# Optimization experiments

Hardware: AMD Instinct MI355X
Metric: run time of the kernel (lower is better)

Reference implementation:

```python
import jax, jax.numpy as jnp
import numpy as np

HEADS = 16
D_MODEL = 1024
EXPANSION = 2
D_EXP = D_MODEL * EXPANSION          # 2048
D_HEAD = D_EXP // HEADS              # 128
B, SEQ = 1, 2048
LN_EPS = 1e-5
NEG_BIG = -1e10


def layer_norm(x, w, b):
    mu = jnp.mean(x, axis=-1, keepdims=True)
    var = jnp.var(x, axis=-1, keepdims=True)
    return (x - mu) * jax.lax.rsqrt(var + LN_EPS) * w + b


def setup_inputs() -> dict:
    key = jax.random.key(0)
    ks = jax.random.split(key, 8)
    d_out = 4 * D_EXP + HEADS  # merged fanout linear: q,k,v,p (D_EXP each) + y (HEADS)
    x = jax.random.normal(ks[0], (B, SEQ, D_MODEL), dtype=jnp.float32)
    W_in = 0.02 * jax.random.normal(ks[1], (d_out, D_MODEL), dtype=jnp.float32)
    b_in = jnp.zeros((d_out,), dtype=jnp.float32)
    # position head init from module: weight zeros, bias linspace(-8,8,heads)
    W_in = W_in.at[4 * D_EXP:].set(0.0)
    b_in = b_in.at[4 * D_EXP:].set(jnp.linspace(-8.0, 8.0, HEADS))
    W_out = 0.02 * (2 * 12) ** (-0.5) * jax.random.normal(ks[2], (D_MODEL, D_EXP), dtype=jnp.float32)
    in_ln_w = jnp.ones((D_MODEL,), dtype=jnp.float32)
    in_ln_b = jnp.zeros((D_MODEL,), dtype=jnp.float32)
    out_ln_w = jnp.ones((D_MODEL,), dtype=jnp.float32)
    out_ln_b = jnp.zeros((D_MODEL,), dtype=jnp.float32)
    smear_factor = jnp.linspace(-6.0, 6.0, HEADS)
    log_scale = jnp.zeros((HEADS,), dtype=jnp.float32)
    return {"x": x, "W_in": W_in, "b_in": b_in, "in_ln_w": in_ln_w, "in_ln_b": in_ln_b,
            "W_out": W_out, "out_ln_w": out_ln_w, "out_ln_b": out_ln_b,
            "smear_factor": smear_factor, "log_scale": log_scale}


def reference(x, W_in, b_in, in_ln_w, in_ln_b, W_out, out_ln_w, out_ln_b, smear_factor, log_scale):
    b, i, d = x.shape
    xn = layer_norm(x, in_ln_w, in_ln_b)
    proj = xn @ W_in.T + b_in  # [b, i, 4*D_EXP + HEADS]
    q, k, v, p, y = jnp.split(proj, [D_EXP, 2 * D_EXP, 3 * D_EXP, 4 * D_EXP], axis=-1)
    to_heads = lambda t: t.reshape(b, i, HEADS, D_HEAD).transpose(0, 2, 1, 3)  # b h i d
    q, k, v = to_heads(q), to_heads(k), to_heads(v)
    # smear mix: k_t <- (1-s)*k_t + s*k_{t-1}
    smear = jax.nn.sigmoid(smear_factor)[None, :, None, None]
    k_prev = jnp.pad(k, ((0, 0), (0, 0), (1, 0), (0, 0)))[:, :, :-1, :]
    k = (1 - smear) * k + smear * k_prev
    s = jnp.exp(log_scale)[None, :, None, None]
    # learned relative positions via cumulative sigmoid
    pos = jnp.cumsum(jax.nn.sigmoid(y).transpose(0, 2, 1), axis=-1)  # [b, h, i]
    relpos = pos[..., :, None] - pos[..., None, :]  # [b, h, i, i]
    causal = jnp.triu(jnp.full((i, i), NEG_BIG, dtype=x.dtype), k=1)
    mask = causal - relpos
    scores = jnp.einsum('bhid,bhjd->bhij', q / s, k / s) / np.sqrt(D_HEAD) + mask
    attn = jax.nn.softmax(scores, axis=-1)
    o = jnp.einsum('bhij,bhjd->bhid', attn, v)
    o = o.transpose(0, 2, 1, 3).reshape(b, i, D_EXP)  # b i (h d)
    out = (jax.nn.silu(p) * o) @ W_out.T
    return layer_norm(out, out_ln_w, out_ln_b)
```

## Files before the change

### kernel.cpp

```cpp
#include <hip/hip_runtime.h>
#include <hip/hip_bf16.h>
#include <cstdint>
#include <cstddef>

#define SEQ    2048
#define DMODEL 1024
#define DEXP   2048
#define NHEADS 16
#define DHEAD  128

typedef __bf16 bf16x8 __attribute__((ext_vector_type(8)));
typedef float  f32x4  __attribute__((ext_vector_type(4)));

__device__ __forceinline__ unsigned short f2bf(float f) {
  unsigned int u = __builtin_bit_cast(unsigned int, f);
  u = u + 0x7FFFu + ((u >> 16) & 1u);
  return (unsigned short)(u >> 16);
}
__device__ __forceinline__ float bf2f(unsigned short h) {
  unsigned int u = ((unsigned int)h) << 16;
  return __builtin_bit_cast(float, u);
}
__device__ __forceinline__ unsigned int pk2bf(float a, float b) {
  return ((unsigned int)f2bf(b) << 16) | f2bf(a);
}

__device__ __forceinline__ void gload_lds16(const void* g, void* l) {
  __builtin_amdgcn_global_load_lds(
      (const __attribute__((address_space(1))) unsigned int*)g,
      (__attribute__((address_space(3))) unsigned int*)l, 16, 0, 0);
}

__global__ __launch_bounds__(256) void ln_kernel(const float* __restrict__ in,
    const float* __restrict__ in2,
    const float* __restrict__ gw, const float* __restrict__ gb,
    unsigned short* __restrict__ out_bf, float* __restrict__ out_f) {
  int row = blockIdx.x, t = threadIdx.x;
  float4 v = reinterpret_cast<const float4*>(in + (size_t)row * DMODEL)[t];
  if (in2) {
    float4 v2 = reinterpret_cast<const float4*>(in2 + (size_t)row * DMODEL)[t];
    v.x += v2.x; v.y += v2.y; v.z += v2.z; v.w += v2.w;
  }
  float s  = v.x + v.y + v.z + v.w;
  float ss = v.x*v.x + v.y*v.y + v.z*v.z + v.w*v.w;
  #pragma unroll
  for (int m = 1; m < 64; m <<= 1) { s += __shfl_xor(s, m, 64); ss += __shfl_xor(ss, m, 64); }
  __shared__ float sh[8];
  if ((t & 63) == 0) { sh[t >> 6] = s; sh[4 + (t >> 6)] = ss; }
  __syncthreads();
  s  = sh[0] + sh[1] + sh[2] + sh[3];
  ss = sh[4] + sh[5] + sh[6] + sh[7];
  float mu  = s * (1.0f / DMODEL);
  float var = ss * (1.0f / DMODEL) - mu * mu;
  float rs  = rsqrtf(var + 1e-5f);
  float4 w4 = reinterpret_cast<const float4*>(gw)[t];
  float4 b4 = reinterpret_cast<const float4*>(gb)[t];
  float o0 = (v.x - mu) * rs * w4.x + b4.x;
  float o1 = (v.y - mu) * rs * w4.y + b4.y;
  float o2 = (v.z - mu) * rs * w4.z + b4.z;
  float o3 = (v.w - mu) * rs * w4.w + b4.w;
  if (out_bf) {
    unsigned short* op = out_bf + (size_t)row * DMODEL + t * 4;
    op[0] = f2bf(o0); op[1] = f2bf(o1); op[2] = f2bf(o2); op[3] = f2bf(o3);
  } else {
    float4 o4; o4.x = o0; o4.y = o1; o4.z = o2; o4.w = o3;
    reinterpret_cast<float4*>(out_f + (size_t)row * DMODEL)[t] = o4;
  }
}

__global__ void castboth(const float* __restrict__ in1, unsigned short* __restrict__ out1,
                         int n1, const float* __restrict__ in2,
                         unsigned short* __restrict__ out2, int n2) {
  int i = blockIdx.x * 256 + threadIdx.x;
  const float* in; unsigned short* out;
  if (i < n1) { in = in1; out = out1; }
  else { i -= n1; if (i >= n2) return; in = in2; out = out2; }
  float4 v = reinterpret_cast<const float4*>(in)[i];
  ushort4 o;
  o.x = f2bf(v.x); o.y = f2bf(v.y); o.z = f2bf(v.z); o.w = f2bf(v.w);
  reinterpret_cast<ushort4*>(out)[i] = o;
}

template<int EPI>
__global__ __launch_bounds__(256) void gemm_lds(
    const unsigned short* __restrict__ A, const unsigned short* __restrict__ B,
    int M, int N, int K,
    const float* __restrict__ b_in, const float* __restrict__ log_scale,
    unsigned short* __restrict__ outq, unsigned short* __restrict__ outk,
    unsigned short* __restrict__ outvt, unsigned short* __restrict__ outp,
    float* __restrict__ outf) {
  int nbn = N / 128;
  int tiles = (M / 128) * nbn;
  int bid = blockIdx.x;
  int part = 0;
  if constexpr (EPI == 1) { part = bid / tiles; bid -= part * tiles; }
  int bm = bid / nbn, bn = bid % nbn;
  int Klen = (EPI == 1) ? (K >> 1) : K;
  int koff = part * Klen;
  int tid = threadIdx.x;
  int wid = tid >> 6, l = tid & 63;
  int wr = wid >> 1, wc = wid & 1;
  int row0 = bm * 128, col0 = bn * 128;
  int c16 = l & 15, g = l >> 4;
  int srow = tid >> 3;
  int sch  = tid & 7;

  __shared__ __align__(16) char SMEM[65536];
  unsigned short* As0 = (unsigned short*)SMEM;
  unsigned short* Bs0 = (unsigned short*)(SMEM + 32768);
  unsigned short* vlds = (unsigned short*)SMEM;

  f32x4 acc[4][4];
  f32x4 z = {0.f, 0.f, 0.f, 0.f};
  #pragma unroll
  for (int i = 0; i < 4; ++i)
    #pragma unroll
    for (int j = 0; j < 4; ++j) acc[i][j] = z;

  auto STAGE = [&](int b, int kt) {
    int k0 = koff + kt * 64;
    #pragma unroll
    for (int rr = 0; rr < 4; ++rr) {
      int row = rr * 32 + srow;
      gload_lds16(A + (size_t)(row0 + row) * K + k0 + sch * 8,
                  (char*)(As0 + b * 8192) + rr * 4096 + tid * 16);
      gload_lds16(B + (size_t)(col0 + row) * K + k0 + sch * 8,
                  (char*)(Bs0 + b * 8192) + rr * 4096 + tid * 16);
    }
  };

  int nkt = Klen >> 6;
  STAGE(0, 0);
  __syncthreads();

  for (int kt = 0; kt < nkt; ++kt) {
    int cur = kt & 1;
    if (kt + 1 < nkt) STAGE(cur ^ 1, kt + 1);
    const unsigned short* Ab = As0 + cur * 8192;
    const unsigned short* Bb = Bs0 + cur * 8192;
    #pragma unroll
    for (int ks = 0; ks < 2; ++ks) {
      bf16x8 a[4], b[4];
      #pragma unroll
      for (int i = 0; i < 4; ++i)
        a[i] = *reinterpret_cast<const bf16x8*>(Ab + (wr * 64 + i * 16 + c16) * 64 + ks * 32 + g * 8);
      #pragma unroll
      for (int j = 0; j < 4; ++j)
        b[j] = *reinterpret_cast<const bf16x8*>(Bb + (wc * 64 + j * 16 + c16) * 64 + ks * 32 + g * 8);
      __builtin_amdgcn_s_setprio(1);
      #pragma unroll
      for (int i = 0; i < 4; ++i)
        #pragma unroll
        for (int j = 0; j < 4; ++j)
          acc[i][j] = __builtin_amdgcn_mfma_f32_16x16x32_bf16(a[i], b[j], acc[i][j], 0, 0, 0);
      __builtin_amdgcn_s_setprio(0);
    }
    __syncthreads();
  }

  if constexpr (EPI == 0) {
    int sec = col0 >> 11;
    if (sec == 2) {
      #pragma unroll
      for (int i = 0; i < 4; ++i)
        #pragma unroll
        for (int j = 0; j < 4; ++j)
          #pragma unroll
          for (int r = 0; r < 4; ++r) {
            int lr = wr * 64 + i * 16 + g * 4 + r;
            int lc = wc * 64 + j * 16 + c16;
            vlds[lr * 130 + lc] = f2bf(acc[i][j][r] + b_in[col0 + lc]);
          }
      __syncthreads();
      int colv0 = col0 & 2047;
      int chunk = tid & 15;
      #pragma unroll
      for (int it = 0; it < 8; ++it) {
        int c = it * 16 + (tid >> 4);
        unsigned short tmp[8];
        #pragma unroll
        for (int e = 0; e < 8; ++e) tmp[e] = vlds[(chunk * 8 + e) * 130 + c];
        *reinterpret_cast<uint4*>(outvt + (size_t)(colv0 + c) * SEQ + row0 + chunk * 8) =
            *reinterpret_cast<const uint4*>(tmp);
      }
      return;
    }
  }

  #pragma unroll
  for (int i = 0; i < 4; ++i) {
    #pragma unroll
    for (int j = 0; j < 4; ++j) {
      #pragma unroll
      for (int r = 0; r < 4; ++r) {
        int gi = row0 + wr * 64 + i * 16 + g * 4 + r;
        int n  = col0 + wc * 64 + j * 16 + c16;
        float val = acc[i][j][r];
        if constexpr (EPI == 0) {
          val += b_in[n];
          int sec = n >> 11, nn = n & 2047, hh = nn >> 7;
          if (sec == 0) {
            float qs = __expf(-2.f * log_scale[hh]) * 0.088388347648318447f;
            outq[(size_t)gi * DEXP + nn] = f2bf(val * qs);
          } else if (sec == 1) {
            outk[(size_t)gi * DEXP + nn] = f2bf(val);
          } else {
            outp[(size_t)gi * DEXP + nn] = f2bf(val);
          }
        } else {
          outf[(size_t)part * M * N + (size_t)gi * N + n] = val;
        }
      }
    }
  }
}

__global__ __launch_bounds__(256) void yproj(const unsigned short* __restrict__ xn,
    const unsigned short* __restrict__ winbf, const float* __restrict__ b_in,
    float* __restrict__ sig_y) {
  int i = blockIdx.x;
  int t = threadIdx.x, wv = t >> 6, l = t & 63;
  const unsigned short* xr = xn + (size_t)i * DMODEL;
  for (int h = wv; h < NHEADS; h += 4) {
    const unsigned short* wr = winbf + (size_t)(4 * DEXP + h) * DMODEL;
    float s = 0.f;
    #pragma unroll
    for (int e = 0; e < 16; ++e) {
      int idx = l + 64 * e;
      s += bf2f(xr[idx]) * bf2f(wr[idx]);
    }
    #pragma unroll
    for (int m = 1; m < 64; m <<= 1) s += __shfl_xor(s, m, 64);
    if (l == 0) {
      float yv = s + b_in[4 * DEXP + h];
      sig_y[h * SEQ + i] = 1.f / (1.f + __expf(-yv));
    }
  }
}

__global__ __launch_bounds__(256) void scan_kernel(const float* __restrict__ sig_y,
                                                   float* __restrict__ pos) {
  int h = blockIdx.x, t = threadIdx.x;
  const float* in = sig_y + (size_t)h * SEQ;
  float v[8], s = 0.f;
  #pragma unroll
  for (int e = 0; e < 8; ++e) { v[e] = in[t * 8 + e]; s += v[e]; }
  __shared__ float sh[256];
  sh[t] = s;
  __syncthreads();
  for (int off = 1; off < 256; off <<= 1) {
    float add = (t >= off) ? sh[t - off] : 0.f;
    __syncthreads();
    sh[t] += add;
    __syncthreads();
  }
  float run = sh[t] - s;
  float* op = pos + (size_t)h * SEQ;
  #pragma unroll
  for (int e = 0; e < 8; ++e) { run += v[e]; op[t * 8 + e] = run; }
}

__global__ void smear_kernel(const unsigned short* __restrict__ projk,
    const float* __restrict__ smearf, unsigned short* __restrict__ ksm) {
  int idx = blockIdx.x * 256 + threadIdx.x;
  if (idx >= SEQ * DEXP) return;
  int i = idx >> 11, nn = idx & 2047, h = nn >> 7;
  float sf = 1.f / (1.f + __expf(-smearf[h]));
  float kc = bf2f(projk[idx]);
  float kp = (i > 0) ? bf2f(projk[idx - DEXP]) : 0.f;
  ksm[idx] = f2bf((1.f - sf) * kc + sf * kp);
}

__global__ __launch_bounds__(256) void attn_kernel(
    const unsigned short* __restrict__ q, const unsigned short* __restrict__ ksm,
    const unsigned short* __restrict__ vt, const unsigned short* __restrict__ projp,
    const float* __restrict__ pos, unsigned short* __restrict__ ap) {
  int bid = blockIdx.x;
  int swz = (bid & 7) * 64 + (bid >> 3);
  int h = swz >> 5;
  int low5 = swz & 31;
  int qc = (h & 1) ? (31 - low5) : low5;
  int q0 = qc * 64;
  int tid = threadIdx.x;
  int w = tid >> 6, l = tid & 63;
  int c16 = l & 15, g = l >> 4;

  __shared__ __align__(16) unsigned short Ks[2][64 * 128];
  __shared__ __align__(16) unsigned short Vs[2][128 * 64];

  int qrow = q0 + w * 16 + c16;
  bf16x8 qf[4];
  {
    const unsigned short* qb = q + (size_t)qrow * DEXP + h * DHEAD + g * 8;
    #pragma unroll
    for (int f = 0; f < 4; ++f) qf[f] = *reinterpret_cast<const bf16x8*>(qb + f * 32);
  }
  float pos_q = pos[h * SEQ + qrow];
  float m_run = -1e30f, l_run = 0.f;
  f32x4 z = {0.f, 0.f, 0.f, 0.f};
  f32x4 oacc[8];
  #pragma unroll
  for (int d = 0; d < 8; ++d) oacc[d] = z;

  int ntiles = qc + 1;
  int kch = tid & 15, krow0 = tid >> 4;
  int vch = tid & 7,  vrow0 = tid >> 3;

  auto STAGE = [&](int b, int t) {
    int j0 = t * 64;
    #pragma unroll
    for (int rr = 0; rr < 4; ++rr) {
      int row = rr * 16 + krow0;
      gload_lds16(ksm + (size_t)(j0 + row) * DEXP + h * DHEAD + ((kch ^ (row & 7)) * 8),
                  (char*)Ks[b] + rr * 4096 + tid * 16);
    }
    #pragma unroll
    for (int rr = 0; rr < 4; ++rr) {
      int row = rr * 32 + vrow0;
      gload_lds16(vt + (size_t)(h * DHEAD + row) * SEQ + j0 + ((vch ^ (row & 7)) * 8),
                  (char*)Vs[b] + rr * 4096 + tid * 16);
    }
  };

  STAGE(0, 0);
  __syncthreads();

  for (int t = 0; t < ntiles; ++t) {
    int cur = t & 1;
    if (t + 1 < ntiles) STAGE(cur ^ 1, t + 1);
    int j0 = t * 64;
    const char* Kb = (const char*)Ks[cur];
    const char* Vb = (const char*)Vs[cur];
    f32x4 sT[4];
    #pragma unroll
    for (int sub = 0; sub < 4; ++sub) {
      sT[sub] = z;
      const char* kb = Kb + (sub * 16 + c16) * 256;
      __builtin_amdgcn_s_setprio(1);
      #pragma unroll
      for (int f = 0; f < 4; ++f) {
        int cb = (f * 64 + g * 16) ^ ((c16 & 7) << 4);
        bf16x8 kf = *reinterpret_cast<const bf16x8*>(kb + cb);
        sT[sub] = __builtin_amdgcn_mfma_f32_16x16x32_bf16(kf, qf[f], sT[sub], 0, 0, 0);
      }
      __builtin_amdgcn_s_setprio(0);
    }
    float a[4][4], mt = -1e30f;
    #pragma unroll
    for (int sub = 0; sub < 4; ++sub) {
      float4 pjv = *reinterpret_cast<const float4*>(pos + h * SEQ + j0 + sub * 16 + g * 4);
      float pj4[4] = { pjv.x, pjv.y, pjv.z, pjv.w };
      #pragma unroll
      for (int r = 0; r < 4; ++r) {
        int j = j0 + sub * 16 + g * 4 + r;
        a[sub][r] = sT[sub][r] - pos_q + pj4[r] + (j > qrow ? -1e10f : 0.f);
        mt = fmaxf(mt, a[sub][r]);
      }
    }
    mt = fmaxf(mt, __shfl_xor(mt, 16, 64));
    mt = fmaxf(mt, __shfl_xor(mt, 32, 64));
    float mn = fmaxf(m_run, mt);
    if (mn - m_run > 8.f) {
      float alpha = __expf(m_run - mn);
      l_run *= alpha;
      #pragma unroll
      for (int d = 0; d < 8; ++d)
        #pragma unroll
        for (int r = 0; r < 4; ++r) oacc[d][r] *= alpha;
      m_run = mn;
    }
    float p[4][4];
    #pragma unroll
    for (int sub = 0; sub < 4; ++sub)
      #pragma unroll
      for (int r = 0; r < 4; ++r) { p[sub][r] = __expf(a[sub][r] - m_run); l_run += p[sub][r]; }
    unsigned long long pk[4];
    #pragma unroll
    for (int sub = 0; sub < 4; ++sub)
      pk[sub] = ((unsigned long long)pk2bf(p[sub][2], p[sub][3]) << 32)
              |  pk2bf(p[sub][0], p[sub][1]);
    int src = c16 + ((g & 1) << 5);
    union { unsigned long long u[2]; bf16x8 v; } pb[2];
    #pragma unroll
    for (int js = 0; js < 2; ++js) {
      unsigned long long t0 = __shfl(pk[2 * js],     src, 64);
      unsigned long long t1 = __shfl(pk[2 * js],     src + 16, 64);
      unsigned long long u0 = __shfl(pk[2 * js + 1], src, 64);
      unsigned long long u1 = __shfl(pk[2 * js + 1], src + 16, 64);
      pb[js].u[0] = (g < 2) ? t0 : u0;
      pb[js].u[1] = (g < 2) ? t1 : u1;
    }
    #pragma unroll
    for (int d = 0; d < 8; ++d) {
      const char* vb = Vb + (d * 16 + c16) * 128;
      __builtin_amdgcn_s_setprio(1);
      #pragma unroll
      for (int js = 0; js < 2; ++js) {
        int cb = (js * 64 + g * 16) ^ ((c16 & 7) << 4);
        bf16x8 vf = *reinterpret_cast<const bf16x8*>(vb + cb);
        oacc[d] = __builtin_amdgcn_mfma_f32_16x16x32_bf16(vf, pb[js].v, oacc[d], 0, 0, 0);
      }
      __builtin_amdgcn_s_setprio(0);
    }
    __syncthreads();
  }

  l_run += __shfl_xor(l_run, 16, 64);
  l_run += __shfl_xor(l_run, 32, 64);
  float inv_l = 1.0f / l_run;
  #pragma unroll
  for (int d = 0; d < 8; ++d) {
    int nn = h * DHEAD + d * 16 + g * 4;
    ushort4 pv4 = *reinterpret_cast<const ushort4*>(projp + (size_t)qrow * DEXP + nn);
    ushort4 o4;
    unsigned short* pvp = reinterpret_cast<unsigned short*>(&pv4);
    unsigned short* op  = reinterpret_cast<unsigned short*>(&o4);
    #pragma unroll
    for (int r = 0; r < 4; ++r) {
      float o = oacc[d][r] * inv_l;
      float pv = bf2f(pvp[r]);
      float si = pv / (1.f + __expf(-pv));
      op[r] = f2bf(si * o);
    }
    *reinterpret_cast<ushort4*>(ap + (size_t)qrow * DEXP + nn) = o4;
  }
}

extern "C" void kernel_launch(void* const* d_in, const int* in_sizes, int n_in,
                              void* d_out, int out_size, void* d_ws, size_t ws_size,
                              hipStream_t stream) {
  const float* x         = (const float*)d_in[0];
  const float* W_in      = (const float*)d_in[1];
  const float* b_in      = (const float*)d_in[2];
  const float* in_ln_w   = (const float*)d_in[3];
  const float* in_ln_b   = (const float*)d_in[4];
  const float* W_out     = (const float*)d_in[5];
  const float* out_ln_w  = (const float*)d_in[6];
  const float* out_ln_b  = (const float*)d_in[7];
  const float* smearf    = (const float*)d_in[8];
  const float* log_scale = (const float*)d_in[9];
  float* out = (float*)d_out;

  char* ws = (char*)d_ws;
  size_t off = 0;
  auto alloc = [&](size_t bytes) -> void* {
    void* p = ws + off;
    off += (bytes + 255) & ~(size_t)255;
    return p;
  };
  unsigned short* xn     = (unsigned short*)alloc((size_t)SEQ * DMODEL * 2);
  unsigned short* winbf  = (unsigned short*)alloc((size_t)(4 * DEXP + NHEADS) * DMODEL * 2);
  unsigned short* woutbf = (unsigned short*)alloc((size_t)DMODEL * DEXP * 2);
  unsigned short* projq  = (unsigned short*)alloc((size_t)SEQ * DEXP * 2);
  unsigned short* projk  = (unsigned short*)alloc((size_t)SEQ * DEXP * 2);
  unsigned short* projp  = (unsigned short*)alloc((size_t)SEQ * DEXP * 2);
  unsigned short* vtb    = (unsigned short*)alloc((size_t)SEQ * DEXP * 2);
  unsigned short* ksm    = (unsigned short*)alloc((size_t)SEQ * DEXP * 2);
  unsigned short* apb    = (unsigned short*)alloc((size_t)SEQ * DEXP * 2);
  float* sig_y = (float*)alloc((size_t)NHEADS * SEQ * 4);
  float* posb  = (float*)alloc((size_t)NHEADS * SEQ * 4);
  float* outf  = (float*)alloc((size_t)2 * SEQ * DMODEL * 4);

  int nwin4  = (4 * DEXP + NHEADS) * DMODEL / 4;
  int nwout4 = DMODEL * DEXP / 4;
  castboth<<<(nwin4 + nwout4 + 255) / 256, 256, 0, stream>>>(
      W_in, winbf, nwin4, W_out, woutbf, nwout4);
  ln_kernel<<<SEQ, 256, 0, stream>>>(x, nullptr, in_ln_w, in_ln_b, xn, nullptr);
  gemm_lds<0><<<(SEQ / 128) * (4 * DEXP / 128), 256, 0, stream>>>(
      xn, winbf, SEQ, 4 * DEXP, DMODEL, b_in, log_scale, projq, projk, vtb, projp, nullptr);
  yproj<<<SEQ, 256, 0, stream>>>(xn, winbf, b_in, sig_y);
  scan_kernel<<<NHEADS, 256, 0, stream>>>(sig_y, posb);
  smear_kernel<<<(SEQ * DEXP + 255) / 256, 256, 0, stream>>>(projk, smearf, ksm);
  attn_kernel<<<512, 256, 0, stream>>>(projq, ksm, vtb, projp, posb, apb);
  gemm_lds<1><<<2 * (SEQ / 128) * (DMODEL / 128), 256, 0, stream>>>(
      apb, woutbf, SEQ, DMODEL, DEXP, nullptr, nullptr, nullptr, nullptr, nullptr, nullptr, outf);
  ln_kernel<<<SEQ, 256, 0, stream>>>(outf, outf + (size_t)SEQ * DMODEL, out_ln_w, out_ln_b,
                                     nullptr, out);
}
```

Baseline: 187.4 us.

## Split attention KV tile across two wave groups and merge softmax partials

The attention block grows from 256 to 512 threads. Two groups of four waves each take one 32-key half of every 64-key tile for the same query rows, and each group keeps its own running max, sum and output accumulator. At the end the partial softmax states are merged through LDS before the silu gating and store. The aim is more waves per block to hide latency and to skip the masked half-tiles on the diagonal, at the cost of an extra LDS merge, a barrier, and higher register and LDS pressure per block.

```diff
diff --git a/kernel.cpp b/kernel.cpp
--- a/kernel.cpp
+++ b/kernel.cpp
@@ -271,7 +271,7 @@
   ksm[idx] = f2bf((1.f - sf) * kc + sf * kp);
 }
 
-__global__ __launch_bounds__(256) void attn_kernel(
+__global__ __launch_bounds__(512) void attn_kernel(
     const unsigned short* __restrict__ q, const unsigned short* __restrict__ ksm,
     const unsigned short* __restrict__ vt, const unsigned short* __restrict__ projp,
     const float* __restrict__ pos, unsigned short* __restrict__ ap) {
@@ -282,13 +282,15 @@
   int qc = (h & 1) ? (31 - low5) : low5;
   int q0 = qc * 64;
   int tid = threadIdx.x;
-  int w = tid >> 6, l = tid & 63;
+  int wid = tid >> 6, l = tid & 63;
+  int w4 = wid & 3, jp = wid >> 2;
+  int joff = jp * 32;
   int c16 = l & 15, g = l >> 4;
 
-  __shared__ __align__(16) unsigned short Ks[2][64 * 128];
-  __shared__ __align__(16) unsigned short Vs[2][128 * 64];
-
-  int qrow = q0 + w * 16 + c16;
+  __shared__ __align__(16) char SMEMa[65536];
+
+  int qrow = q0 + w4 * 16 + c16;
+  int wmax = q0 + w4 * 16 + 15;
   bf16x8 qf[4];
   {
     const unsigned short* qb = q + (size_t)qrow * DEXP + h * DHEAD + g * 8;
@@ -309,16 +311,16 @@
   auto STAGE = [&](int b, int t) {
     int j0 = t * 64;
     #pragma unroll
-    for (int rr = 0; rr < 4; ++rr) {
-      int row = rr * 16 + krow0;
+    for (int rr = 0; rr < 2; ++rr) {
+      int row = rr * 32 + krow0;
       gload_lds16(ksm + (size_t)(j0 + row) * DEXP + h * DHEAD + ((kch ^ (row & 7)) * 8),
-                  (char*)Ks[b] + rr * 4096 + tid * 16);
-    }
-    #pragma unroll
-    for (int rr = 0; rr < 4; ++rr) {
-      int row = rr * 32 + vrow0;
+                  SMEMa + b * 16384 + rr * 8192 + tid * 16);
+    }
+    #pragma unroll
+    for (int rr = 0; rr < 2; ++rr) {
+      int row = rr * 64 + vrow0;
       gload_lds16(vt + (size_t)(h * DHEAD + row) * SEQ + j0 + ((vch ^ (row & 7)) * 8),
-                  (char*)Vs[b] + rr * 4096 + tid * 16);
+                  SMEMa + 32768 + b * 16384 + rr * 8192 + tid * 16);
     }
   };
 
@@ -329,100 +331,116 @@
     int cur = t & 1;
     if (t + 1 < ntiles) STAGE(cur ^ 1, t + 1);
     int j0 = t * 64;
-    const char* Kb = (const char*)Ks[cur];
-    const char* Vb = (const char*)Vs[cur];
-    f32x4 sT[4];
-    #pragma unroll
-    for (int sub = 0; sub < 4; ++sub) {
-      sT[sub] = z;
-      const char* kb = Kb + (sub * 16 + c16) * 256;
-      __builtin_amdgcn_s_setprio(1);
-      #pragma unroll
-      for (int f = 0; f < 4; ++f) {
-        int cb = (f * 64 + g * 16) ^ ((c16 & 7) << 4);
-        bf16x8 kf = *reinterpret_cast<const bf16x8*>(kb + cb);
-        sT[sub] = __builtin_amdgcn_mfma_f32_16x16x32_bf16(kf, qf[f], sT[sub], 0, 0, 0);
-      }
-      __builtin_amdgcn_s_setprio(0);
-    }
-    float a[4][4], mt = -1e30f;
-    #pragma unroll
-    for (int sub = 0; sub < 4; ++sub) {
-      float4 pjv = *reinterpret_cast<const float4*>(pos + h * SEQ + j0 + sub * 16 + g * 4);
-      float pj4[4] = { pjv.x, pjv.y, pjv.z, pjv.w };
-      #pragma unroll
-      for (int r = 0; r < 4; ++r) {
-        int j = j0 + sub * 16 + g * 4 + r;
-        a[sub][r] = sT[sub][r] - pos_q + pj4[r] + (j > qrow ? -1e10f : 0.f);
-        mt = fmaxf(mt, a[sub][r]);
-      }
-    }
-    mt = fmaxf(mt, __shfl_xor(mt, 16, 64));
-    mt = fmaxf(mt, __shfl_xor(mt, 32, 64));
-    float mn = fmaxf(m_run, mt);
-    if (mn - m_run > 8.f) {
-      float alpha = __expf(m_run - mn);
-      l_run *= alpha;
-      #pragma unroll
-      for (int d = 0; d < 8; ++d)
-        #pragma unroll
-        for (int r = 0; r < 4; ++r) oacc[d][r] *= alpha;
-      m_run = mn;
-    }
-    float p[4][4];
-    #pragma unroll
-    for (int sub = 0; sub < 4; ++sub)
-      #pragma unroll
-      for (int r = 0; r < 4; ++r) { p[sub][r] = __expf(a[sub][r] - m_run); l_run += p[sub][r]; }
-    unsigned long long pk[4];
-    #pragma unroll
-    for (int sub = 0; sub < 4; ++sub)
-      pk[sub] = ((unsigned long long)pk2bf(p[sub][2], p[sub][3]) << 32)
-              |  pk2bf(p[sub][0], p[sub][1]);
-    int src = c16 + ((g & 1) << 5);
-    union { unsigned long long u[2]; bf16x8 v; } pb[2];
-    #pragma unroll
-    for (int js = 0; js < 2; ++js) {
-      unsigned long long t0 = __shfl(pk[2 * js],     src, 64);
-      unsigned long long t1 = __shfl(pk[2 * js],     src + 16, 64);
-      unsigned long long u0 = __shfl(pk[2 * js + 1], src, 64);
-      unsigned long long u1 = __shfl(pk[2 * js + 1], src + 16, 64);
-      pb[js].u[0] = (g < 2) ? t0 : u0;
-      pb[js].u[1] = (g < 2) ? t1 : u1;
-    }
-    #pragma unroll
-    for (int d = 0; d < 8; ++d) {
-      const char* vb = Vb + (d * 16 + c16) * 128;
-      __builtin_amdgcn_s_setprio(1);
-      #pragma unroll
-      for (int js = 0; js < 2; ++js) {
-        int cb = (js * 64 + g * 16) ^ ((c16 & 7) << 4);
+    if (j0 + joff <= wmax) {
+      const char* Kb = SMEMa + cur * 16384;
+      const char* Vb = SMEMa + 32768 + cur * 16384;
+      f32x4 sT[2];
+      #pragma unroll
+      for (int sub = 0; sub < 2; ++sub) {
+        sT[sub] = z;
+        const char* kb = Kb + (joff + sub * 16 + c16) * 256;
+        __builtin_amdgcn_s_setprio(1);
+        #pragma unroll
+        for (int f = 0; f < 4; ++f) {
+          int cb = (f * 64 + g * 16) ^ ((c16 & 7) << 4);
+          bf16x8 kf = *reinterpret_cast<const bf16x8*>(kb + cb);
+          sT[sub] = __builtin_amdgcn_mfma_f32_16x16x32_bf16(kf, qf[f], sT[sub], 0, 0, 0);
+        }
+        __builtin_amdgcn_s_setprio(0);
+      }
+      float a[2][4], mt = -1e30f;
+      #pragma unroll
+      for (int sub = 0; sub < 2; ++sub) {
+        float4 pjv = *reinterpret_cast<const float4*>(pos + h * SEQ + j0 + joff + sub * 16 + g * 4);
+        float pj4[4] = { pjv.x, pjv.y, pjv.z, pjv.w };
+        #pragma unroll
+        for (int r = 0; r < 4; ++r) {
+          int j = j0 + joff + sub * 16 + g * 4 + r;
+          a[sub][r] = sT[sub][r] - pos_q + pj4[r] + (j > qrow ? -1e10f : 0.f);
+          mt = fmaxf(mt, a[sub][r]);
+        }
+      }
+      mt = fmaxf(mt, __shfl_xor(mt, 16, 64));
+      mt = fmaxf(mt, __shfl_xor(mt, 32, 64));
+      float mn = fmaxf(m_run, mt);
+      if (mn - m_run > 8.f) {
+        float alpha = __expf(m_run - mn);
+        l_run *= alpha;
+        #pragma unroll
+        for (int d = 0; d < 8; ++d)
+          #pragma unroll
+          for (int r = 0; r < 4; ++r) oacc[d][r] *= alpha;
+        m_run = mn;
+      }
+      float p[2][4];
+      #pragma unroll
+      for (int sub = 0; sub < 2; ++sub)
+        #pragma unroll
+        for (int r = 0; r < 4; ++r) { p[sub][r] = __expf(a[sub][r] - m_run); l_run += p[sub][r]; }
+      unsigned long long pk0 = ((unsigned long long)pk2bf(p[0][2], p[0][3]) << 32)
+                             |  pk2bf(p[0][0], p[0][1]);
+      unsigned long long pk1 = ((unsigned long long)pk2bf(p[1][2], p[1][3]) << 32)
+                             |  pk2bf(p[1][0], p[1][1]);
+      int src = c16 + ((g & 1) << 5);
+      unsigned long long t0 = __shfl(pk0, src, 64);
+      unsigned long long t1 = __shfl(pk0, src + 16, 64);
+      unsigned long long u0 = __shfl(pk1, src, 64);
+      unsigned long long u1 = __shfl(pk1, src + 16, 64);
+      union { unsigned long long u[2]; bf16x8 v; } pb;
+      pb.u[0] = (g < 2) ? t0 : u0;
+      pb.u[1] = (g < 2) ? t1 : u1;
+      #pragma unroll
+      for (int d = 0; d < 8; ++d) {
+        const char* vb = Vb + (d * 16 + c16) * 128;
+        int cb = (joff * 2 + g * 16) ^ ((c16 & 7) << 4);
         bf16x8 vf = *reinterpret_cast<const bf16x8*>(vb + cb);
-        oacc[d] = __builtin_amdgcn_mfma_f32_16x16x32_bf16(vf, pb[js].v, oacc[d], 0, 0, 0);
-      }
-      __builtin_amdgcn_s_setprio(0);
+        __builtin_amdgcn_s_setprio(1);
+        oacc[d] = __builtin_amdgcn_mfma_f32_16x16x32_bf16(vf, pb.v, oacc[d], 0, 0, 0);
+        __builtin_amdgcn_s_setprio(0);
+      }
     }
     __syncthreads();
   }
 
   l_run += __shfl_xor(l_run, 16, 64);
   l_run += __shfl_xor(l_run, 32, 64);
-  float inv_l = 1.0f / l_run;
-  #pragma unroll
-  for (int d = 0; d < 8; ++d) {
-    int nn = h * DHEAD + d * 16 + g * 4;
-    ushort4 pv4 = *reinterpret_cast<const ushort4*>(projp + (size_t)qrow * DEXP + nn);
-    ushort4 o4;
-    unsigned short* pvp = reinterpret_cast<unsigned short*>(&pv4);
-    unsigned short* op  = reinterpret_cast<unsigned short*>(&o4);
-    #pragma unroll
-    for (int r = 0; r < 4; ++r) {
-      float o = oacc[d][r] * inv_l;
-      float pv = bf2f(pvp[r]);
-      float si = pv / (1.f + __expf(-pv));
-      op[r] = f2bf(si * o);
-    }
-    *reinterpret_cast<ushort4*>(ap + (size_t)qrow * DEXP + nn) = o4;
+
+  float* mbuf = (float*)SMEMa;
+  float* obuf = (float*)(SMEMa + 1024);
+  if (jp == 0) {
+    if (g == 0) {
+      mbuf[(w4 * 2 + 0) * 16 + c16] = m_run;
+      mbuf[(w4 * 2 + 1) * 16 + c16] = l_run;
+    }
+    #pragma unroll
+    for (int d = 0; d < 8; ++d)
+      #pragma unroll
+      for (int r = 0; r < 4; ++r)
+        obuf[(w4 * 16 + c16) * 132 + d * 16 + g * 4 + r] = oacc[d][r];
+  }
+  __syncthreads();
+  if (jp == 1) {
+    float m0 = mbuf[(w4 * 2 + 0) * 16 + c16];
+    float l0 = mbuf[(w4 * 2 + 1) * 16 + c16];
+    float M = fmaxf(m0, m_run);
+    float s0 = __expf(m0 - M), s1 = __expf(m_run - M);
+    float invl = 1.0f / (l0 * s0 + l_run * s1);
+    #pragma unroll
+    for (int d = 0; d < 8; ++d) {
+      int nn = h * DHEAD + d * 16 + g * 4;
+      ushort4 pv4 = *reinterpret_cast<const ushort4*>(projp + (size_t)qrow * DEXP + nn);
+      ushort4 o4;
+      unsigned short* pvp = reinterpret_cast<unsigned short*>(&pv4);
+      unsigned short* op  = reinterpret_cast<unsigned short*>(&o4);
+      #pragma unroll
+      for (int r = 0; r < 4; ++r) {
+        float o = (obuf[(w4 * 16 + c16) * 132 + d * 16 + g * 4 + r] * s0 + oacc[d][r] * s1) * invl;
+        float pv = bf2f(pvp[r]);
+        float si = pv / (1.f + __expf(-pv));
+        op[r] = f2bf(si * o);
+      }
+      *reinterpret_cast<ushort4*>(ap + (size_t)qrow * DEXP + nn) = o4;
+    }
   }
 }
 
@@ -471,7 +489,7 @@
   yproj<<<SEQ, 256, 0, stream>>>(xn, winbf, b_in, sig_y);
   scan_kernel<<<NHEADS, 256, 0, stream>>>(sig_y, posb);
   smear_kernel<<<(SEQ * DEXP + 255) / 256, 256, 0, stream>>>(projk, smearf, ksm);
-  attn_kernel<<<512, 256, 0, stream>>>(projq, ksm, vtb, projp, posb, apb);
+  attn_kernel<<<512, 512, 0, stream>>>(projq, ksm, vtb, projp, posb, apb);
   gemm_lds<1><<<2 * (SEQ / 128) * (DMODEL / 128), 256, 0, stream>>>(
       apb, woutbf, SEQ, DMODEL, DEXP, nullptr, nullptr, nullptr, nullptr, nullptr, nullptr, outf);
   ln_kernel<<<SEQ, 256, 0, stream>>>(outf, outf + (size_t)SEQ * DMODEL, out_ln_w, out_ln_b,
```

Result: faster. 169.2 us (-9.7%).
